# Kernel optimization log

Measured on AMD Instinct MI355X. Metric: run time of the kernel, lower is better.

## Reference

```python
import jax, jax.numpy as jnp
import numpy as np

B, TD, TC = 64, 800, 80
ENC, H, MA, MO = 128, 400, 10, 20
OUT = MO * 6 + 1  # 121


def _lstm(x, h0, c0, Wih, Whh, bih, bhh):
    # x: (B,T,I); PyTorch gate order i,f,g,o
    xg = jnp.einsum('bti,gi->btg', x, Wih) + (bih + bhh)  # (B,T,4H)
    def step(carry, xg_t):
        h, c = carry
        g = xg_t + h @ Whh.T
        i, f, gg, o = jnp.split(g, 4, axis=-1)
        c = jax.nn.sigmoid(f) * c + jax.nn.sigmoid(i) * jnp.tanh(gg)
        h = jax.nn.sigmoid(o) * jnp.tanh(c)
        return (h, c), h
    (_, _), hs = jax.lax.scan(step, (h0, c0), xg.transpose(1, 0, 2))
    return hs.transpose(1, 0, 2)  # (B,T,H)


def setup_inputs() -> dict:
    key = jax.random.key(0)
    ks = jax.random.split(key, 16)
    s = 0.05
    rn = lambda k, sh, sc=1.0: jax.random.normal(k, sh, jnp.float32) * sc
    I1 = 3 + ENC + H
    return {
        'strokes': rn(ks[0], (B, TD, 3)),
        'context': rn(ks[1], (B, TC, ENC)),
        'context_mask': jnp.ones((B, TC), jnp.float32),
        'h_0': rn(ks[2], (3, 2 * H), s),
        'Wih0': rn(ks[3], (4 * H, 3), s), 'Whh0': rn(ks[4], (4 * H, H), s),
        'bih0': jnp.zeros((4 * H,), jnp.float32), 'bhh0': jnp.zeros((4 * H,), jnp.float32),
        'Wih1': rn(ks[5], (4 * H, I1), s), 'Whh1': rn(ks[6], (4 * H, H), s),
        'bih1': jnp.zeros((4 * H,), jnp.float32), 'bhh1': jnp.zeros((4 * H,), jnp.float32),
        'Wih2': rn(ks[7], (4 * H, I1), s), 'Whh2': rn(ks[8], (4 * H, H), s),
        'bih2': jnp.zeros((4 * H,), jnp.float32), 'bhh2': jnp.zeros((4 * H,), jnp.float32),
        'attn_W': rn(ks[9], (3 * MA, H), s), 'attn_b': jnp.zeros((3 * MA,), jnp.float32),
        'out_W': rn(ks[10], (OUT, 3 * H), s), 'out_b': jnp.zeros((OUT,), jnp.float32),
    }


def reference(strokes, context, context_mask, h_0,
              Wih0, Whh0, bih0, bhh0,
              Wih1, Whh1, bih1, bhh1,
              Wih2, Whh2, bih2, bhh2,
              attn_W, attn_b, out_W, out_b):
    bsz = strokes.shape[0]
    # initial states: h_0[l] split into (h, c)
    init = [(jnp.broadcast_to(h_0[l, :H], (bsz, H)), jnp.broadcast_to(h_0[l, H:], (bsz, H))) for l in range(3)]

    h0s = _lstm(strokes, init[0][0], init[0][1], Wih0, Whh0, bih0, bhh0)  # (B,TD,H)

    # Gaussian monotonic attention
    p = jnp.exp(h0s @ attn_W.T + attn_b)  # (B,TD,3MA)
    alpha, beta, kappa = jnp.split(p, 3, axis=-1)
    kappa = jnp.cumsum(0.2 * kappa, axis=1)  # (B,TD,MA)
    u = jnp.arange(TC, dtype=jnp.float32)  # (TC,)
    # phi: (B,TD,TC)
    diff = kappa[:, :, None, :] - u[None, None, :, None]
    phi = jnp.sum(alpha[:, :, None, :] * jnp.exp(-beta[:, :, None, :] * diff * diff), axis=-1)
    w = jnp.einsum('btu,bue->bte', phi * context_mask[:, None, :], context)  # (B,TD,ENC)

    x1 = jnp.concatenate([strokes, h0s, w], axis=2)
    h1s = _lstm(x1, init[1][0], init[1][1], Wih1, Whh1, bih1, bhh1)
    x2 = jnp.concatenate([strokes, h1s, w], axis=2)
    h2s = _lstm(x2, init[2][0], init[2][1], Wih2, Whh2, bih2, bhh2)

    outputs = jnp.concatenate([h0s, h1s, h2s], axis=-1) @ out_W.T + out_b  # (B,TD,121)
    return outputs
```

## Files before the change

kernel.cpp:

```cpp
#include <hip/hip_runtime.h>
#include <stdint.h>

typedef unsigned short u16;
typedef __attribute__((ext_vector_type(8))) short bf16x8;
typedef __attribute__((ext_vector_type(4))) float f32x4;
typedef __attribute__((ext_vector_type(4))) int   i32x4;
typedef __attribute__((ext_vector_type(4))) unsigned short u16x4;

#define DI static __device__ __forceinline__

constexpr int B_   = 64;
constexpr int TD   = 800;
constexpr int TC   = 80;
constexpr int ENC  = 128;
constexpr int H    = 400;
constexpr int OUTN = 121;

constexpr int HP   = 416;
constexpr int KT_H = 13;
constexpr int KOP  = 1216;
constexpr int NOP  = 128;
constexpr int NBL  = 25;
constexpr int NBA  = 32;
constexpr int CSTR = 32;
constexpr int FSLOT= 32;

constexpr size_t HB_B  = (size_t)(TD+1)*B_*HP*2;
constexpr size_t WBF_B = (size_t)TD*B_*ENC*2;
constexpr size_t STR_B = (size_t)TD*B_*4*4;
constexpr size_t APK_B = (size_t)NBL*4*KT_H*64*8*2;
constexpr size_t WF_B  = (size_t)NBL*4*17*64*8*2;

constexpr size_t OFF_HB0 = 0;
constexpr size_t OFF_HB1 = OFF_HB0 + HB_B;
constexpr size_t OFF_HB2 = OFF_HB1 + HB_B;
constexpr size_t OFF_HLO = OFF_HB2 + HB_B;
constexpr size_t OFF_WBF = OFF_HLO + HB_B;
constexpr size_t OFF_STR = OFF_WBF + WBF_B;
constexpr size_t OFF_APKH= OFF_STR + STR_B;
constexpr size_t OFF_APKL= OFF_APKH + 3*APK_B;
constexpr size_t OFF_WF1 = OFF_APKL + APK_B;
constexpr size_t OFF_WF2 = OFF_WF1 + WF_B;
constexpr size_t OFF_OUW = OFF_WF2 + WF_B;
constexpr size_t OFF_BIA = OFF_OUW + (size_t)NOP*KOP*2;
constexpr size_t OFF_CNT = OFF_BIA + (size_t)3*1600*4;
constexpr size_t WS_NEED = OFF_CNT + (size_t)4*FSLOT*CSTR*4 + 256;

constexpr int LDS_DUMP = 0;
constexpr int LDS_CL   = 66560;
constexpr int LDS_EX   = 70656;
constexpr int LDS_W3   = 140288;
constexpr int LDS_BIAS = 141056;
constexpr int LDSB     = 141312;
constexpr int ALDS_CTX = 0;
constexpr int ALDS_ATW = 81920;
constexpr int ALDS_H   = 130040;
constexpr int ALDS_PHI = 133240;
constexpr int ALDS_MSK = 133880;
constexpr int ALDS_KAP = 134520;
constexpr int ALDS_P   = 134600;

DI u16 f2b(float f){ union{float f; unsigned u;} v; v.f=f; unsigned r = v.u + 0x7FFFu + ((v.u>>16)&1u); return (u16)(r>>16); }
DI float b2f(u16 h){ union{unsigned u; float f;} v; v.u=((unsigned)h)<<16; return v.f; }
DI float sigm(float x){ return 1.f/(1.f+__expf(-x)); }
DI float tanh_(float x){ float a=fabsf(x), e=__expf(-2.f*a), t=(1.f-e)/(1.f+e); return x<0.f ? -t : t; }

DI void st16(u16* p, u16 v){
  asm volatile("global_store_short %0, %1, off sc0 sc1" :: "v"(p), "v"((unsigned)v) : "memory");
}
DI void st8(u16* p, u16x4 v){
  unsigned long long x; __builtin_memcpy(&x, &v, 8);
  asm volatile("global_store_dwordx2 %0, %1, off sc0 sc1" :: "v"(p), "v"(x) : "memory");
}
DI void setflag(unsigned* p, unsigned t){
  asm volatile("global_store_dword %0, %1, off sc0 sc1" :: "v"(p), "v"(t) : "memory");
}
DI void waitflags2(const unsigned* fA, int nA, unsigned tA,
                   const unsigned* fB, int nB, unsigned tB){
  int lane = threadIdx.x & 63;
  const unsigned* p; unsigned tgt;
  if (lane < nA)            { p = fA + (size_t)lane*CSTR;        tgt = tA; }
  else if (lane < nA+nB)    { p = fB + (size_t)(lane-nA)*CSTR;   tgt = tB; }
  else                      { p = fA;                            tgt = 0;  }
  while (1) {
    unsigned v = __hip_atomic_load(p, __ATOMIC_RELAXED, __HIP_MEMORY_SCOPE_AGENT);
    if (__all(v >= tgt)) break;
    __builtin_amdgcn_s_sleep(1);
  }
  asm volatile("" ::: "memory");
}

__global__ void k_init(const float* __restrict__ h0, u16* hb0, u16* hb1, u16* hb2, u16* hlo,
                       unsigned* cnt){
  int i = blockIdx.x*256 + threadIdx.x;
  const int nA = 3*B_*HP, nA2 = B_*HP, nB = 4*TD*B_*16, nC = 4*FSLOT;
  if (i < nA) {
    int l = i/(B_*HP); int rem = i - l*(B_*HP); int b = rem/HP; int k = rem - b*HP;
    u16 v = (k<H) ? f2b(h0[l*800 + k]) : (u16)0;
    (l==0?hb0:(l==1?hb1:hb2))[(size_t)b*HP + k] = v;
  } else if (i < nA+nA2) {
    int rem = i - nA; int b = rem/HP; int k = rem - b*HP;
    u16 v = 0;
    if (k < H) { float w = h0[k]; u16 hi = f2b(w); v = f2b(w - b2f(hi)); }
    hlo[(size_t)b*HP + k] = v;
  } else if (i < nA+nA2+nB) {
    int q = i - nA - nA2; int buf = q/(TD*B_*16); int r2 = q % (TD*B_*16);
    int t = r2/(B_*16) + 1; int r3 = r2 % (B_*16); int b = r3>>4; int kk = r3&15;
    u16* hb = (buf==0)?hb0:((buf==1)?hb1:((buf==2)?hb2:hlo));
    hb[((size_t)t*B_ + b)*HP + 400 + kk] = 0;
  } else if (i < nA+nA2+nB+nC) {
    int q = i - nA - nA2 - nB;
    cnt[(size_t)q*CSTR] = 0u;
  }
}

__global__ void k_apack(const float* W0, const float* W1, const float* W2,
                        u16* apkHi, u16* apkLo){
  int i = blockIdx.x*256 + threadIdx.x;
  const int total = 3*NBL*4*KT_H*64;
  if (i >= total) return;
  int lane = i & 63; int r = i >> 6;
  int kt = r % KT_H; r /= KT_H;
  int mt = r % 4;    r /= 4;
  int j  = r % NBL;  int lv = r / NBL;
  const float* W = (lv==0)?W0:((lv==1)?W1:W2);
  int row = mt*400 + j*16 + (lane & 15);
  int kbase = kt*32 + (lane>>4)*8;
  #pragma unroll
  for (int e=0;e<8;++e){
    int k = kbase+e;
    float w = (k<H) ? W[(size_t)row*H + k] : 0.f;
    u16 hi = f2b(w);
    apkHi[(size_t)i*8 + e] = hi;
    if (lv == 0) apkLo[(size_t)i*8 + e] = f2b(w - b2f(hi));
  }
}

__global__ void k_wihpack2(const float* __restrict__ W, u16* __restrict__ dst){
  int i = blockIdx.x*256 + threadIdx.x;
  if (i >= NBL*4*17*64) return;
  int lane = i & 63; int r = i >> 6;
  int ktf = r % 17; r /= 17; int mt = r % 4; int j = r / 4;
  int row = mt*400 + j*16 + (lane & 15);
  int kbase = ktf*32 + (lane>>4)*8;
  #pragma unroll
  for (int e=0;e<8;++e){
    int k = kbase+e;
    int col;
    if (ktf < 13) col = (k < 400) ? (3 + k) : -1;
    else          col = 403 + (k - 416);
    dst[(size_t)i*8 + e] = (col >= 0) ? f2b(W[(size_t)row*531 + col]) : (u16)0;
  }
}

__global__ void k_smallpack(const float* outW,
                            const float* bi0, const float* bh0, const float* bi1, const float* bh1,
                            const float* bi2, const float* bh2,
                            u16* ouw, float* biasP){
  int i = blockIdx.x*256 + threadIdx.x;
  const int n2 = NOP*KOP, n3 = 3*1600;
  if (i < n2) {
    int n = i/KOP, k = i - n*KOP;
    ouw[i] = (n<OUTN && k<1200) ? f2b(outW[(size_t)n*1200 + k]) : (u16)0;
  } else if (i < n2+n3) {
    int q = i-n2; int l = q/1600, row = q - l*1600;
    const float* bi = (l==0)?bi0:((l==1)?bi1:bi2);
    const float* bh = (l==0)?bh0:((l==1)?bh1:bh2);
    biasP[q] = bi[row] + bh[row];
  }
}

__global__ void k_packs(const float* __restrict__ strokes, float* __restrict__ st){
  int i = blockIdx.x*256 + threadIdx.x;
  if (i >= TD*B_) return;
  int t = i / B_, b = i & 63;
  st[(size_t)i*4+0] = strokes[((size_t)b*TD + t)*3 + 0];
  st[(size_t)i*4+1] = strokes[((size_t)b*TD + t)*3 + 1];
  st[(size_t)i*4+2] = strokes[((size_t)b*TD + t)*3 + 2];
  st[(size_t)i*4+3] = 0.f;
}

template<int L>
DI void stage_lstm(char* smem, int j,
    const u16* __restrict__ apkHi,
    const u16* __restrict__ exG,
    const float* __restrict__ strokesT,
    const float* __restrict__ wihRaw, int wihStride,
    const float* __restrict__ biasL,
    const float* __restrict__ h0g,
    u16* __restrict__ hb_self, const u16* __restrict__ hb_prev,
    u16* __restrict__ hlo_, const u16* __restrict__ wbf,
    unsigned* __restrict__ fSelf, const unsigned* __restrict__ fDep, int nDep)
{
  float* dumpS = (float*)(smem + LDS_DUMP);
  float* cL    = (float*)(smem + LDS_CL);
  u16*   exS   = (u16*)  (smem + LDS_EX);
  float* w3S   = (float*)(smem + LDS_W3);
  float* biasS = (float*)(smem + LDS_BIAS);
  const int tid = threadIdx.x, wv = tid>>6, l = tid&63;
  const int col = l&15, kg = l>>4;

  bf16x8 ahi[4][4];
  #pragma unroll
  for (int mt=0;mt<4;++mt)
    #pragma unroll
    for (int i=0;i<4;++i){
      int kt = wv + i*4;
      if (kt < KT_H) ahi[mt][i] = *(const bf16x8*)(apkHi + (size_t)j*26624 + ((size_t)(mt*KT_H + kt)*64 + l)*8);
      else { bf16x8 z = {0,0,0,0,0,0,0,0}; ahi[mt][i] = z; }
    }
  {
    const int nv = (L==0) ? 3328 : 4352;
    const size_t stride = (L==0) ? 26624 : 34816;
    const i32x4* src = (const i32x4*)(exG + (size_t)j*stride);
    i32x4* dst = (i32x4*)exS;
    for (int i = tid; i < nv; i += 256) dst[i] = src[i];
  }
  if (tid < 192) {
    int local = tid/3, c = tid - (tid/3)*3;
    int row = (local>>4)*400 + j*16 + (local&15);
    w3S[tid] = wihRaw[(size_t)row*wihStride + c];
  }
  if (tid < 64) {
    int row = (tid>>4)*400 + j*16 + (tid&15);
    biasS[tid] = biasL[row];
  }
  for (int i = tid; i < 1024; i += 256) cL[i] = h0g[L*800 + 400 + j*16 + (i>>6)];
  __syncthreads();

  for (int t = 1; t <= TD; ++t) {
    if constexpr (L > 0) waitflags2(fDep, nDep, (unsigned)t, fSelf, NBL, (unsigned)(t-1));
    else                 waitflags2(fSelf, NBL, (unsigned)(t-1), nullptr, 0, 0u);
    f32x4 acc[4][4];
    #pragma unroll
    for (int mt=0;mt<4;++mt)
      #pragma unroll
      for (int nt=0;nt<4;++nt){ f32x4 z = {0.f,0.f,0.f,0.f}; acc[mt][nt] = z; }

    const u16* hbase = hb_self + (size_t)(t-1)*B_*HP + kg*8;
    const u16* lbase = (L==0) ? (hlo_ + (size_t)(t-1)*B_*HP + kg*8) : nullptr;
    #pragma unroll
    for (int i=0;i<4;++i){
      int kt = wv + i*4;
      if (kt < KT_H) {
        bf16x8 bhi[4], blo[4];
        #pragma unroll
        for (int nt=0;nt<4;++nt){
          bhi[nt] = *(const bf16x8*)(hbase + (size_t)(nt*16+col)*HP + kt*32);
          if constexpr (L==0) blo[nt] = *(const bf16x8*)(lbase + (size_t)(nt*16+col)*HP + kt*32);
        }
        #pragma unroll
        for (int mt=0;mt<4;++mt){
          bf16x8 a = ahi[mt][i];
          #pragma unroll
          for (int nt=0;nt<4;++nt)
            acc[mt][nt] = __builtin_amdgcn_mfma_f32_16x16x32_bf16(a, bhi[nt], acc[mt][nt], 0,0,0);
          if constexpr (L==0) {
            bf16x8 al = *(const bf16x8*)(exS + ((size_t)(mt*KT_H + kt)*64 + l)*8);
            #pragma unroll
            for (int nt=0;nt<4;++nt){
              acc[mt][nt] = __builtin_amdgcn_mfma_f32_16x16x32_bf16(a,  blo[nt], acc[mt][nt], 0,0,0);
              acc[mt][nt] = __builtin_amdgcn_mfma_f32_16x16x32_bf16(al, bhi[nt], acc[mt][nt], 0,0,0);
            }
          }
        }
      }
    }
    if constexpr (L > 0) {
      const u16* pbase = hb_prev + (size_t)t*B_*HP + kg*8;
      const u16* wbase = wbf + ((size_t)(t-1)*B_)*ENC + kg*8;
      #pragma unroll
      for (int i=0;i<5;++i){
        int ktf = wv + i*4;
        if (ktf < 17) {
          bf16x8 bfr[4];
          if (ktf < 13) {
            #pragma unroll
            for (int nt=0;nt<4;++nt) bfr[nt] = *(const bf16x8*)(pbase + (size_t)(nt*16+col)*HP + ktf*32);
          } else {
            #pragma unroll
            for (int nt=0;nt<4;++nt) bfr[nt] = *(const bf16x8*)(wbase + (size_t)(nt*16+col)*ENC + (ktf-13)*32);
          }
          #pragma unroll
          for (int mt=0;mt<4;++mt){
            bf16x8 a = *(const bf16x8*)(exS + ((size_t)(mt*17 + ktf)*64 + l)*8);
            #pragma unroll
            for (int nt=0;nt<4;++nt)
              acc[mt][nt] = __builtin_amdgcn_mfma_f32_16x16x32_bf16(a, bfr[nt], acc[mt][nt], 0,0,0);
          }
        }
      }
    }
    #pragma unroll
    for (int mt=0;mt<4;++mt)
      #pragma unroll
      for (int nt=0;nt<4;++nt)
        #pragma unroll
        for (int r=0;r<4;++r)
          dumpS[wv*4160 + (mt*16 + kg*4 + r)*65 + nt*16 + col] = acc[mt][nt][r];
    __syncthreads();
    {
      const int bg = tid & 63, uq = tid >> 6;
      const float* sp = strokesT + ((size_t)(t-1)*B_ + bg)*4;
      float sx = sp[0], sy = sp[1], sz = sp[2];
      u16x4 hh4, ll4;
      #pragma unroll
      for (int e=0;e<4;++e){
        int u = uq*4 + e;
        int idx = u*64 + bg;
        float gv[4];
        #pragma unroll
        for (int g=0; g<4; ++g){
          int row = g*16 + u;
          float s = dumpS[row*65 + bg] + dumpS[4160 + row*65 + bg]
                  + dumpS[8320 + row*65 + bg] + dumpS[12480 + row*65 + bg];
          s += biasS[row] + w3S[row*3+0]*sx + w3S[row*3+1]*sy + w3S[row*3+2]*sz;
          gv[g] = s;
        }
        float co = cL[idx];
        float i_ = sigm(gv[0]), f_ = sigm(gv[1]), g_ = tanh_(gv[2]), o_ = sigm(gv[3]);
        float cn = f_*co + i_*g_;
        cL[idx] = cn;
        float hv = o_*tanh_(cn);
        u16 hh = f2b(hv);
        hh4[e] = hh;
        if constexpr (L==0) ll4[e] = f2b(hv - b2f(hh));
      }
      st8(hb_self + ((size_t)t*B_ + bg)*HP + j*16 + uq*4, hh4);
      if constexpr (L==0) st8(hlo_ + ((size_t)t*B_ + bg)*HP + j*16 + uq*4, ll4);
    }
    __syncthreads();
    if (tid == 0) setflag(fSelf + (size_t)j*CSTR, (unsigned)t);
  }
}

DI void stage_attn(char* smem, int j2,
    const float* __restrict__ ctx, const float* __restrict__ cmask,
    const float* __restrict__ attnW, const float* __restrict__ attnB,
    const u16* __restrict__ hb0, const u16* __restrict__ hlo_,
    u16* __restrict__ wbf,
    const unsigned* __restrict__ fA, unsigned* __restrict__ fB)
{
  float* ctxS = (float*)(smem + ALDS_CTX);
  float* atwS = (float*)(smem + ALDS_ATW);
  float* hS   = (float*)(smem + ALDS_H);
  float* phiS = (float*)(smem + ALDS_PHI);
  float* mskS = (float*)(smem + ALDS_MSK);
  float* kapS = (float*)(smem + ALDS_KAP);
  float* pS   = (float*)(smem + ALDS_P);
  const int tid = threadIdx.x;
  const int b0 = j2*2;
  for (int i = tid; i < 2*80*128; i += 256) {
    int bi = i/10240, rem = i%10240;
    ctxS[i] = ctx[(size_t)(b0+bi)*10240 + rem];
  }
  for (int i = tid; i < 30*400; i += 256) {
    int row = i/400, k = i - row*400;
    atwS[row*401 + k] = attnW[i];
  }
  for (int i = tid; i < 160; i += 256) {
    int bi = i/80, u = i - bi*80;
    mskS[i] = cmask[(b0+bi)*80 + u];
  }
  if (tid < 20) kapS[tid] = 0.f;
  float aB = (tid < 60) ? attnB[tid % 30] : 0.f;
  __syncthreads();

  for (int t = 1; t <= TD; ++t) {
    waitflags2(fA, NBL, (unsigned)t, nullptr, 0, 0u);
    if (tid < 200) {
      int bi = tid/100, k = (tid%100)*4;
      size_t off = ((size_t)t*B_ + (b0+bi))*HP + k;
      u16x4 hi4 = *(const u16x4*)(hb0 + off);
      u16x4 lo4 = *(const u16x4*)(hlo_ + off);
      #pragma unroll
      for (int e=0;e<4;++e) hS[bi*400 + k + e] = b2f(hi4[e]) + b2f(lo4[e]);
    }
    __syncthreads();
    if (tid < 60) {
      int bi = tid/30, row = tid - bi*30;
      const float* ar = atwS + row*401;
      const float* hr = hS + bi*400;
      float a0=0,a1=0,a2=0,a3=0;
      for (int k=0;k<400;k+=4){
        a0 += ar[k]*hr[k]; a1 += ar[k+1]*hr[k+1];
        a2 += ar[k+2]*hr[k+2]; a3 += ar[k+3]*hr[k+3];
      }
      pS[bi*30+row] = __expf(a0+a1+a2+a3 + aB);
    }
    __syncthreads();
    if (tid < 20) {
      int bi = tid/10, m = tid - bi*10;
      kapS[tid] += 0.2f * pS[bi*30 + 20 + m];
    }
    __syncthreads();
    if (tid < 160) {
      int bi = tid/80; float u2 = (float)(tid - bi*80);
      const float* pb = pS + bi*30; const float* kb = kapS + bi*10;
      float a = 0.f;
      #pragma unroll
      for (int m=0;m<10;++m){ float d = kb[m]-u2; a += pb[m]*__expf(-pb[10+m]*d*d); }
      phiS[tid] = a * mskS[tid];
    }
    __syncthreads();
    {
      int bi = tid >> 7, e = tid & 127;
      const float* ph = phiS + bi*80;
      const float* cs = ctxS + (size_t)bi*10240 + e;
      float a = 0.f;
      for (int u = 0; u < TC; ++u) a += ph[u]*cs[u*128];
      st16(wbf + ((size_t)(t-1)*B_ + (b0+bi))*ENC + e, f2b(a));
    }
    __syncthreads();
    if (tid == 0) setflag(fB + (size_t)j2*CSTR, (unsigned)t);
  }
}

__global__ __launch_bounds__(256,1) void k_mega(
    const u16* apkH, const u16* apkL, const u16* wf1, const u16* wf2,
    const float* strokesT, const float* Wih0, const float* Wih1, const float* Wih2,
    const float* bia, const float* h0g,
    u16* hb0, u16* hb1, u16* hb2, u16* hlo, u16* wbf,
    const float* ctx, const float* cmask, const float* attnW, const float* attnB,
    unsigned* cnt)
{
  extern __shared__ char smem[];
  unsigned* fA = cnt;
  unsigned* fB = cnt + (size_t)FSLOT*CSTR;
  unsigned* fC = cnt + (size_t)2*FSLOT*CSTR;
  unsigned* fD = cnt + (size_t)3*FSLOT*CSTR;
  int j = blockIdx.x;
  if (j < NBL) {
    stage_lstm<0>(smem, j, apkH, apkL, strokesT, Wih0, 3, bia, h0g,
                  hb0, nullptr, hlo, nullptr, fA, nullptr, 0);
  } else if (j < NBL+NBA) {
    stage_attn(smem, j-NBL, ctx, cmask, attnW, attnB, hb0, hlo, wbf, fA, fB);
  } else if (j < 2*NBL+NBA) {
    stage_lstm<1>(smem, j-NBL-NBA, apkH + (size_t)1*NBL*26624, wf1, strokesT, Wih1, 531,
                  bia+1600, h0g, hb1, hb0, nullptr, wbf, fC, fB, NBA);
  } else {
    stage_lstm<2>(smem, j-2*NBL-NBA, apkH + (size_t)2*NBL*26624, wf2, strokesT, Wih2, 531,
                  bia+3200, h0g, hb2, hb1, nullptr, wbf, fD, fC, NBL);
  }
}

__global__ __launch_bounds__(256) void k_gemm_out(const u16* __restrict__ hb0, const u16* __restrict__ hb1,
                                                  const u16* __restrict__ hb2, const u16* __restrict__ ouw,
                                                  const float* __restrict__ out_b, float* __restrict__ dout){
  int wv = threadIdx.x>>6, l = threadIdx.x&63;
  int task = blockIdx.x*4 + wv;
  int ng = task & 1; int mpair = task >> 1;
  int m0 = mpair*32; int t = m0>>6; int broff = m0 & 63;
  int col = l&15, kg = l>>4;
  f32x4 acc[2][4];
  #pragma unroll
  for (int mt=0;mt<2;++mt)
    #pragma unroll
    for (int nt=0;nt<4;++nt){ f32x4 z = {0.f,0.f,0.f,0.f}; acc[mt][nt] = z; }
  for (int kt=0; kt<38; ++kt) {
    int k0 = kt*32 + kg*8;
    int reg = (k0>=800) ? 2 : ((k0>=400) ? 1 : 0);
    int koff = k0 - reg*400;
    const u16* hb = (reg==0) ? hb0 : ((reg==1) ? hb1 : hb2);
    bf16x8 afr[2];
    #pragma unroll
    for (int mt=0;mt<2;++mt)
      afr[mt] = *(const bf16x8*)(hb + ((size_t)(t+1)*B_ + broff + mt*16 + col)*HP + koff);
    #pragma unroll
    for (int nt=0;nt<4;++nt) {
      bf16x8 bfr = *(const bf16x8*)(ouw + (size_t)(ng*64 + nt*16 + col)*KOP + k0);
      #pragma unroll
      for (int mt=0;mt<2;++mt)
        acc[mt][nt] = __builtin_amdgcn_mfma_f32_16x16x32_bf16(afr[mt], bfr, acc[mt][nt], 0,0,0);
    }
  }
  #pragma unroll
  for (int mt=0;mt<2;++mt)
    #pragma unroll
    for (int nt=0;nt<4;++nt)
      #pragma unroll
      for (int r=0;r<4;++r) {
        int n = ng*64 + nt*16 + col;
        int bo = broff + mt*16 + kg*4 + r;
        if (n < OUTN) dout[((size_t)bo*TD + t)*OUTN + n] = acc[mt][nt][r] + out_b[n];
      }
}

__global__ void k_sentinel(float* o, float code){ o[threadIdx.x] = code; }

extern "C" void kernel_launch(void* const* d_in, const int* in_sizes, int n_in,
                              void* d_out, int out_size, void* d_ws, size_t ws_size,
                              hipStream_t stream) {
  const float* strokes = (const float*)d_in[0];
  const float* context = (const float*)d_in[1];
  const float* cmask   = (const float*)d_in[2];
  const float* h0      = (const float*)d_in[3];
  const float* Wih0 = (const float*)d_in[4];  const float* Whh0 = (const float*)d_in[5];
  const float* bih0 = (const float*)d_in[6];  const float* bhh0 = (const float*)d_in[7];
  const float* Wih1 = (const float*)d_in[8];  const float* Whh1 = (const float*)d_in[9];
  const float* bih1 = (const float*)d_in[10]; const float* bhh1 = (const float*)d_in[11];
  const float* Wih2 = (const float*)d_in[12]; const float* Whh2 = (const float*)d_in[13];
  const float* bih2 = (const float*)d_in[14]; const float* bhh2 = (const float*)d_in[15];
  const float* attnW = (const float*)d_in[16]; const float* attnB = (const float*)d_in[17];
  const float* outW  = (const float*)d_in[18]; const float* outB  = (const float*)d_in[19];
  float* dout = (float*)d_out;

  if (ws_size < WS_NEED) {
    float code = 1000.0f + (float)(ws_size >> 20);
    k_sentinel<<<1, 64, 0, stream>>>(dout, code);
    return;
  }

  char* ws = (char*)d_ws;
  u16* hb0 = (u16*)(ws + OFF_HB0);
  u16* hb1 = (u16*)(ws + OFF_HB1);
  u16* hb2 = (u16*)(ws + OFF_HB2);
  u16* hlo = (u16*)(ws + OFF_HLO);
  u16* wbf = (u16*)(ws + OFF_WBF);
  float* strT = (float*)(ws + OFF_STR);
  u16* apkH = (u16*)(ws + OFF_APKH);
  u16* apkL = (u16*)(ws + OFF_APKL);
  u16* wf1  = (u16*)(ws + OFF_WF1);
  u16* wf2  = (u16*)(ws + OFF_WF2);
  u16* ouw  = (u16*)(ws + OFF_OUW);
  float* bia = (float*)(ws + OFF_BIA);
  unsigned* cnt = (unsigned*)(ws + OFF_CNT);

  (void)hipFuncSetAttribute((const void*)k_mega, hipFuncAttributeMaxDynamicSharedMemorySize, LDSB);

  {
    int n = 3*B_*HP + B_*HP + 4*TD*B_*16 + 4*FSLOT;
    k_init<<<(n+255)/256, 256, 0, stream>>>(h0, hb0, hb1, hb2, hlo, cnt);
  }
  k_apack<<<(3*NBL*4*KT_H*64+255)/256, 256, 0, stream>>>(Whh0, Whh1, Whh2, apkH, apkL);
  k_wihpack2<<<(NBL*4*17*64+255)/256, 256, 0, stream>>>(Wih1, wf1);
  k_wihpack2<<<(NBL*4*17*64+255)/256, 256, 0, stream>>>(Wih2, wf2);
  {
    int n = NOP*KOP + 3*1600;
    k_smallpack<<<(n+255)/256, 256, 0, stream>>>(outW, bih0,bhh0,bih1,bhh1,bih2,bhh2, ouw, bia);
  }
  k_packs<<<(TD*B_+255)/256, 256, 0, stream>>>(strokes, strT);

  k_mega<<<2*NBL+NBA+NBL, 256, LDSB, stream>>>(apkH, apkL, wf1, wf2,
      strT, Wih0, Wih1, Wih2, bia, h0,
      hb0, hb1, hb2, hlo, wbf,
      context, cmask, attnW, attnB, cnt);

  k_gemm_out<<<3200/4, 256, 0, stream>>>(hb0, hb1, hb2, ouw, outB, dout);
}
```

Baseline: 7.840 ms.

## Pack sync flags contiguously and split attention projection across more threads

Per-block progress flags move from a 128-byte stride to a dense array, so a polling wave fetches all flags in a few cache lines instead of one line per lane. The attention-parameter dot products are split into four 100-element segments across 240 threads, with the partial sums reduced in LDS before the exp. The cost is one extra barrier per timestep, and flags written by different blocks now share cache lines, which can cause contention between writers.

```diff
diff --git a/kernel.cpp b/kernel.cpp
--- a/kernel.cpp
+++ b/kernel.cpp
@@ -22,7 +22,7 @@
 constexpr int NOP  = 128;
 constexpr int NBL  = 25;
 constexpr int NBA  = 32;
-constexpr int CSTR = 32;
+constexpr int CSTR = 1;
 constexpr int FSLOT= 32;
 
 constexpr size_t HB_B  = (size_t)(TD+1)*B_*HP*2;
@@ -44,7 +44,7 @@
 constexpr size_t OFF_OUW = OFF_WF2 + WF_B;
 constexpr size_t OFF_BIA = OFF_OUW + (size_t)NOP*KOP*2;
 constexpr size_t OFF_CNT = OFF_BIA + (size_t)3*1600*4;
-constexpr size_t WS_NEED = OFF_CNT + (size_t)4*FSLOT*CSTR*4 + 256;
+constexpr size_t WS_NEED = OFF_CNT + (size_t)4*FSLOT*4 + 256;
 
 constexpr int LDS_DUMP = 0;
 constexpr int LDS_CL   = 66560;
@@ -59,6 +59,7 @@
 constexpr int ALDS_MSK = 133880;
 constexpr int ALDS_KAP = 134520;
 constexpr int ALDS_P   = 134600;
+constexpr int ALDS_PPS = 134840;
 
 DI u16 f2b(float f){ union{float f; unsigned u;} v; v.f=f; unsigned r = v.u + 0x7FFFu + ((v.u>>16)&1u); return (u16)(r>>16); }
 DI float b2f(u16 h){ union{unsigned u; float f;} v; v.u=((unsigned)h)<<16; return v.f; }
@@ -79,9 +80,9 @@
                    const unsigned* fB, int nB, unsigned tB){
   int lane = threadIdx.x & 63;
   const unsigned* p; unsigned tgt;
-  if (lane < nA)            { p = fA + (size_t)lane*CSTR;        tgt = tA; }
-  else if (lane < nA+nB)    { p = fB + (size_t)(lane-nA)*CSTR;   tgt = tB; }
-  else                      { p = fA;                            tgt = 0;  }
+  if (lane < nA)            { p = fA + lane;        tgt = tA; }
+  else if (lane < nA+nB)    { p = fB + (lane-nA);   tgt = tB; }
+  else                      { p = fA;               tgt = 0;  }
   while (1) {
     unsigned v = __hip_atomic_load(p, __ATOMIC_RELAXED, __HIP_MEMORY_SCOPE_AGENT);
     if (__all(v >= tgt)) break;
@@ -110,7 +111,7 @@
     hb[((size_t)t*B_ + b)*HP + 400 + kk] = 0;
   } else if (i < nA+nA2+nB+nC) {
     int q = i - nA - nA2 - nB;
-    cnt[(size_t)q*CSTR] = 0u;
+    cnt[q] = 0u;
   }
 }
 
@@ -330,7 +331,7 @@
       if constexpr (L==0) st8(hlo_ + ((size_t)t*B_ + bg)*HP + j*16 + uq*4, ll4);
     }
     __syncthreads();
-    if (tid == 0) setflag(fSelf + (size_t)j*CSTR, (unsigned)t);
+    if (tid == 0) setflag(fSelf + j, (unsigned)t);
   }
 }
 
@@ -348,6 +349,7 @@
   float* mskS = (float*)(smem + ALDS_MSK);
   float* kapS = (float*)(smem + ALDS_KAP);
   float* pS   = (float*)(smem + ALDS_P);
+  float* ppsS = (float*)(smem + ALDS_PPS);
   const int tid = threadIdx.x;
   const int b0 = j2*2;
   for (int i = tid; i < 2*80*128; i += 256) {
@@ -377,16 +379,24 @@
       for (int e=0;e<4;++e) hS[bi*400 + k + e] = b2f(hi4[e]) + b2f(lo4[e]);
     }
     __syncthreads();
-    if (tid < 60) {
-      int bi = tid/30, row = tid - bi*30;
-      const float* ar = atwS + row*401;
-      const float* hr = hS + bi*400;
+    if (tid < 240) {
+      int bi = tid/120, r = tid - bi*120;
+      int row = r>>2, seg = r&3;
+      const float* ar = atwS + row*401 + seg*100;
+      const float* hr = hS + bi*400 + seg*100;
       float a0=0,a1=0,a2=0,a3=0;
-      for (int k=0;k<400;k+=4){
+      #pragma unroll 4
+      for (int k=0;k<100;k+=4){
         a0 += ar[k]*hr[k]; a1 += ar[k+1]*hr[k+1];
         a2 += ar[k+2]*hr[k+2]; a3 += ar[k+3]*hr[k+3];
       }
-      pS[bi*30+row] = __expf(a0+a1+a2+a3 + aB);
+      ppsS[(bi*30+row)*4+seg] = a0+a1+a2+a3;
+    }
+    __syncthreads();
+    if (tid < 60) {
+      int bi = tid/30, row = tid - bi*30;
+      const float* pp = ppsS + (bi*30+row)*4;
+      pS[bi*30+row] = __expf(pp[0]+pp[1]+pp[2]+pp[3] + aB);
     }
     __syncthreads();
     if (tid < 20) {
@@ -412,7 +422,7 @@
       st16(wbf + ((size_t)(t-1)*B_ + (b0+bi))*ENC + e, f2b(a));
     }
     __syncthreads();
-    if (tid == 0) setflag(fB + (size_t)j2*CSTR, (unsigned)t);
+    if (tid == 0) setflag(fB + j2, (unsigned)t);
   }
 }
 
@@ -426,9 +436,9 @@
 {
   extern __shared__ char smem[];
   unsigned* fA = cnt;
-  unsigned* fB = cnt + (size_t)FSLOT*CSTR;
-  unsigned* fC = cnt + (size_t)2*FSLOT*CSTR;
-  unsigned* fD = cnt + (size_t)3*FSLOT*CSTR;
+  unsigned* fB = cnt + FSLOT;
+  unsigned* fC = cnt + 2*FSLOT;
+  unsigned* fD = cnt + 3*FSLOT;
   int j = blockIdx.x;
   if (j < NBL) {
     stage_lstm<0>(smem, j, apkH, apkL, strokesT, Wih0, 3, bia, h0g,
```

After: 9.015 ms. 15.0% more time.
